# Kernel optimization log

Measured on AMD Instinct MI355X. Metric: run time of the kernel, lower is better.

Reference implementation:

```python
import jax, jax.numpy as jnp
import numpy as np

D_MODEL = 1024
N_HEADS = 16
D_HEAD = D_MODEL // N_HEADS


def setup_inputs() -> dict:
    key = jax.random.key(0)
    ks = jax.random.split(key, 7)
    x = jax.random.normal(ks[0], (1, 4096, D_MODEL), dtype=jnp.float32)
    # torch Linear default init ~ U(-1/sqrt(fan_in), 1/sqrt(fan_in)); small randn is fine for a reference
    Wqkv = jax.random.normal(ks[1], (3 * D_MODEL, D_MODEL), dtype=jnp.float32) * (1.0 / np.sqrt(D_MODEL))
    bqkv = jax.random.normal(ks[2], (3 * D_MODEL,), dtype=jnp.float32) * 0.01
    Wo = jax.random.normal(ks[3], (D_MODEL, D_MODEL), dtype=jnp.float32) * (1.0 / np.sqrt(D_MODEL))
    bo = jax.random.normal(ks[4], (D_MODEL,), dtype=jnp.float32) * 0.01
    wq = jnp.ones((D_HEAD,), dtype=jnp.float32)
    wk = jnp.ones((D_HEAD,), dtype=jnp.float32)
    return {"x": x, "Wqkv": Wqkv, "bqkv": bqkv, "Wo": Wo, "bo": bo, "wq": wq, "wk": wk}


def _rmsnorm(x, w):
    # matches RMSNormRef: mean of squares over last dim, eps added to mean before sqrt
    xf = x.astype(jnp.float32)
    rms = jnp.mean(xf * xf, axis=-1, keepdims=True)
    return (xf / jnp.sqrt(rms + 1e-6) * w.astype(jnp.float32)).astype(x.dtype)


def reference(x, Wqkv, bqkv, Wo, bo, wq, wk):
    b, s, d = x.shape
    qkv = x @ Wqkv.T + bqkv                       # [b, s, 3d]
    q, k, v = jnp.split(qkv, 3, axis=-1)
    q = q.reshape(b, s, N_HEADS, D_HEAD)
    k = k.reshape(b, s, N_HEADS, D_HEAD)
    v = v.reshape(b, s, N_HEADS, D_HEAD)
    q = _rmsnorm(q, wq)
    k = _rmsnorm(k, wk)
    # NOTE: original applies NO 1/sqrt(d_head) scaling and NO causal mask
    qf = q.astype(jnp.float32)
    kf = k.astype(jnp.float32)
    vf = v.astype(jnp.float32)
    attn = jnp.einsum('bqhd,bkhd->bhqk', qf, kf)  # [b, h, s, s] fp32 scores
    attn = jax.nn.softmax(attn, axis=-1)
    z = jnp.einsum('bhqk,bkhd->bqhd', attn, vf).astype(x.dtype)
    z = z.reshape(b, s, d)
    return z @ Wo.T + bo
```

## Files before the change

kernel.cpp:

```cpp
#include <hip/hip_runtime.h>
#include <hip/hip_bf16.h>

typedef __bf16 bf16;
typedef bf16 bf16x8 __attribute__((ext_vector_type(8)));
typedef bf16 bf16x4 __attribute__((ext_vector_type(4)));
typedef float f32x4 __attribute__((ext_vector_type(4)));
typedef float f32x16 __attribute__((ext_vector_type(16)));
typedef unsigned int u32;
typedef u32 u32x4 __attribute__((ext_vector_type(4)));

static constexpr int SEQ    = 4096;
static constexpr int DMODEL = 1024;
static constexpr int NHEADS = 16;
static constexpr int DHEAD  = 64;
static constexpr int QKV3   = 3 * DMODEL;
static constexpr float SMAX = 64.0f;
static constexpr float LOG2E = 1.44269504088896341f;

__device__ inline void gld16(const bf16* g, bf16* l) {
    __builtin_amdgcn_global_load_lds(
        (const __attribute__((address_space(1))) void*)g,
        (__attribute__((address_space(3))) void*)l, 16, 0, 0);
}

__device__ inline bf16x8 load8(const float* src) {
    float4 a = *(const float4*)(src);
    float4 b = *(const float4*)(src + 4);
    bf16x8 r;
    r[0] = (bf16)a.x; r[1] = (bf16)a.y; r[2] = (bf16)a.z; r[3] = (bf16)a.w;
    r[4] = (bf16)b.x; r[5] = (bf16)b.y; r[6] = (bf16)b.z; r[7] = (bf16)b.w;
    return r;
}

__device__ inline f32x16 zero16() {
    f32x16 r;
#pragma unroll
    for (int i = 0; i < 16; ++i) r[i] = 0.f;
    return r;
}

static constexpr size_t NX = (size_t)SEQ * DMODEL;
static constexpr size_t NW = (size_t)QKV3 * DMODEL;
static constexpr size_t NO = (size_t)DMODEL * DMODEL;

__global__ __launch_bounds__(256)
void cvt_all(const float* __restrict__ x, const float* __restrict__ Wqkv,
             const float* __restrict__ Wo, bf16* __restrict__ outbase) {
    const size_t e = ((size_t)blockIdx.x * 256 + threadIdx.x) * 8;
    const float* src;
    if (e < NX)            src = x + e;
    else if (e < NX + NW)  src = Wqkv + (e - NX);
    else                   src = Wo + (e - NX - NW);
    *(bf16x8*)(outbase + e) = load8(src);
}

__global__ __launch_bounds__(256)
void gemm_qkv(const bf16* __restrict__ A, const bf16* __restrict__ W,
              const float* __restrict__ bias, const float* __restrict__ wq,
              const float* __restrict__ wk, bf16* __restrict__ qkv,
              bf16* __restrict__ Vt) {
    __shared__ __align__(16) bf16 As[128 * 32];
    __shared__ __align__(16) bf16 Ws[128 * 32];
    const int tid  = threadIdx.x;
    const int wave = tid >> 6;
    const int ll   = tid & 15;
    const int quad = (tid & 63) >> 4;
    const int wm   = (wave >> 1) * 64;
    const int wn   = (wave & 1) * 64;
    const int m0 = blockIdx.y * 128;
    const int n0 = blockIdx.x * 128;

    f32x4 acc[4][4];
#pragma unroll
    for (int i = 0; i < 4; ++i)
#pragma unroll
        for (int j = 0; j < 4; ++j) acc[i][j] = (f32x4){0.f, 0.f, 0.f, 0.f};

    for (int k0 = 0; k0 < DMODEL; k0 += 32) {
        __syncthreads();
#pragma unroll
        for (int i = 0; i < 2; ++i) {
            const int idx = i * 256 + tid;
            const int row = idx >> 2;
            const int c   = (idx & 3) ^ ((row >> 1) & 3);
            gld16(&A[(size_t)(m0 + row) * DMODEL + k0 + c * 8], As + idx * 8);
            gld16(&W[(size_t)(n0 + row) * DMODEL + k0 + c * 8], Ws + idx * 8);
        }
        __syncthreads();
        bf16x8 af[4], bfr[4];
#pragma unroll
        for (int mi = 0; mi < 4; ++mi) {
            const int row = wm + mi * 16 + ll;
            af[mi] = *(const bf16x8*)(As + (row * 4 + (quad ^ ((ll >> 1) & 3))) * 8);
        }
#pragma unroll
        for (int ni = 0; ni < 4; ++ni) {
            const int row = wn + ni * 16 + ll;
            bfr[ni] = *(const bf16x8*)(Ws + (row * 4 + (quad ^ ((ll >> 1) & 3))) * 8);
        }
#pragma unroll
        for (int mi = 0; mi < 4; ++mi)
#pragma unroll
            for (int ni = 0; ni < 4; ++ni)
                acc[mi][ni] = __builtin_amdgcn_mfma_f32_16x16x32_bf16(
                    af[mi], bfr[ni], acc[mi][ni], 0, 0, 0);
    }

    float bvn[4];
#pragma unroll
    for (int ni = 0; ni < 4; ++ni) bvn[ni] = bias[n0 + wn + ni * 16 + ll];

    const int sect = (n0 + wn) >> 10;
    if (sect < 2) {
        const float* wv = sect ? wk : wq;
        float wvl[4];
#pragma unroll
        for (int ni = 0; ni < 4; ++ni) wvl[ni] = wv[ni * 16 + ll];
#pragma unroll
        for (int mi = 0; mi < 4; ++mi)
#pragma unroll
            for (int r = 0; r < 4; ++r) {
                float xf[4];
                float ss = 0.f;
#pragma unroll
                for (int ni = 0; ni < 4; ++ni) {
                    xf[ni] = (float)(bf16)(acc[mi][ni][r] + bvn[ni]);
                    ss += xf[ni] * xf[ni];
                }
#pragma unroll
                for (int off = 1; off < 16; off <<= 1) ss += __shfl_xor(ss, off);
                const float scale = rsqrtf(ss * (1.0f / 64.0f) + 1e-6f);
                const int row = m0 + wm + mi * 16 + quad * 4 + r;
#pragma unroll
                for (int ni = 0; ni < 4; ++ni)
                    qkv[(size_t)row * QKV3 + n0 + wn + ni * 16 + ll] =
                        (bf16)(xf[ni] * scale * wvl[ni]);
            }
    } else {
        const int h = (n0 + wn - 2 * DMODEL) >> 6;
#pragma unroll
        for (int mi = 0; mi < 4; ++mi) {
            const int kv = m0 + wm + mi * 16 + quad * 4;
#pragma unroll
            for (int ni = 0; ni < 4; ++ni) {
                bf16x4 vv;
#pragma unroll
                for (int r = 0; r < 4; ++r) vv[r] = (bf16)(acc[mi][ni][r] + bvn[ni]);
                *(bf16x4*)(Vt + (size_t)(h * DHEAD + ni * 16 + ll) * SEQ + kv) = vv;
            }
        }
    }
}

__global__ __launch_bounds__(256)
void gemm_out(const bf16* __restrict__ A, const bf16* __restrict__ W,
              const float* __restrict__ bias, float* __restrict__ C) {
    __shared__ __align__(16) bf16 As[128 * 32];
    __shared__ __align__(16) bf16 Ws[64 * 32];
    const int tid  = threadIdx.x;
    const int wave = tid >> 6;
    const int ll   = tid & 15;
    const int quad = (tid & 63) >> 4;
    const int m0 = blockIdx.y * 128;
    const int n0 = blockIdx.x * 64;

    f32x4 acc[2][4];
#pragma unroll
    for (int i = 0; i < 2; ++i)
#pragma unroll
        for (int j = 0; j < 4; ++j) acc[i][j] = (f32x4){0.f, 0.f, 0.f, 0.f};

    for (int k0 = 0; k0 < DMODEL; k0 += 32) {
        __syncthreads();
#pragma unroll
        for (int i = 0; i < 2; ++i) {
            const int idx = i * 256 + tid;
            const int row = idx >> 2;
            const int c   = (idx & 3) ^ ((row >> 1) & 3);
            gld16(&A[(size_t)(m0 + row) * DMODEL + k0 + c * 8], As + idx * 8);
        }
        {
            const int j   = tid;
            const int row = j >> 2;
            const int c   = (j & 3) ^ ((row >> 1) & 3);
            gld16(&W[(size_t)(n0 + row) * DMODEL + k0 + c * 8], Ws + j * 8);
        }
        __syncthreads();
        bf16x8 af[2], bfr[4];
#pragma unroll
        for (int mi = 0; mi < 2; ++mi) {
            const int row = wave * 32 + mi * 16 + ll;
            af[mi] = *(const bf16x8*)(As + (row * 4 + (quad ^ ((ll >> 1) & 3))) * 8);
        }
#pragma unroll
        for (int ni = 0; ni < 4; ++ni) {
            const int row = ni * 16 + ll;
            bfr[ni] = *(const bf16x8*)(Ws + (row * 4 + (quad ^ ((ll >> 1) & 3))) * 8);
        }
#pragma unroll
        for (int mi = 0; mi < 2; ++mi)
#pragma unroll
            for (int ni = 0; ni < 4; ++ni)
                acc[mi][ni] = __builtin_amdgcn_mfma_f32_16x16x32_bf16(
                    af[mi], bfr[ni], acc[mi][ni], 0, 0, 0);
    }
#pragma unroll
    for (int ni = 0; ni < 4; ++ni) {
        const int col = n0 + ni * 16 + ll;
        const float bv = bias[col];
#pragma unroll
        for (int mi = 0; mi < 2; ++mi)
#pragma unroll
            for (int r = 0; r < 4; ++r) {
                const int row = m0 + wave * 32 + mi * 16 + quad * 4 + r;
                C[(size_t)row * DMODEL + col] = acc[mi][ni][r] + bv;
            }
    }
}

template<bool PARTIAL>
__global__ __launch_bounds__(256, 4)
void attn_fwd(const bf16* __restrict__ qkv, const bf16* __restrict__ Vt,
              bf16* __restrict__ z, float* __restrict__ opf,
              float* __restrict__ lsum) {
    __shared__ __align__(16) bf16 KV[2][2][64 * 64];
    float (*Os)[32][36] = (float(*)[32][36])(&KV[0][0][0]);
    bf16* Qs = &KV[1][0][0];

    const int tid  = threadIdx.x;
    const int wave = tid >> 6;
    const int lane = tid & 63;
    const int l31  = lane & 31;
    const int hh   = lane >> 5;
    const int l7   = lane & 7;
    const int head = blockIdx.x;
    const int q0   = blockIdx.y * 128;
    const int half = PARTIAL ? blockIdx.z : 0;
    const int kvbeg = half * (SEQ / 2);
    const int kvlen = PARTIAL ? (SEQ / 2) : SEQ;
    const int nt    = kvlen / 64;

    const bf16* kbase  = qkv + DMODEL + head * DHEAD;
    const bf16* vtbase = Vt + (size_t)head * DHEAD * SEQ;

    auto stage_kv = [&](int buf, int kv0) {
#pragma unroll
        for (int i = 0; i < 2; ++i) {
            const int idx = i * 256 + tid;
            const int row = idx >> 3;
            const int c   = (idx & 7) ^ (row & 7);
            gld16(kbase + (size_t)(kv0 + row) * QKV3 + c * 8, &KV[buf][0][0] + idx * 8);
            gld16(vtbase + (size_t)row * SEQ + kv0 + c * 8, &KV[buf][1][0] + idx * 8);
        }
    };

#pragma unroll
    for (int i = 0; i < 4; ++i) {
        const int idx = i * 256 + tid;
        const int row = idx >> 3;
        const int c   = (idx & 7) ^ (row & 7);
        gld16(qkv + (size_t)(q0 + row) * QKV3 + head * DHEAD + c * 8, Qs + idx * 8);
    }
    stage_kv(0, kvbeg);
    __syncthreads();

    bf16x8 qf[4];
#pragma unroll
    for (int kd = 0; kd < 4; ++kd)
        qf[kd] = *(const bf16x8*)(Qs + ((wave * 32 + l31) * 8 + ((kd * 2 + hh) ^ l7)) * 8);
    __syncthreads();

    f32x16 o[2];
    o[0] = zero16();
    o[1] = zero16();
    float lpa[4] = {0.f, 0.f, 0.f, 0.f};

    int cur = 0;
    for (int t = 0; t < nt; ++t) {
        if (t + 1 < nt) stage_kv(cur ^ 1, kvbeg + (t + 1) * 64);
        const bf16* Ks  = &KV[cur][0][0];
        const bf16* VTs = &KV[cur][1][0];

        f32x16 st0 = zero16(), st1 = zero16();
        __builtin_amdgcn_s_setprio(1);
#pragma unroll
        for (int kd = 0; kd < 4; ++kd) {
            bf16x8 kf = *(const bf16x8*)(Ks + ((l31) * 8 + ((kd * 2 + hh) ^ l7)) * 8);
            st0 = __builtin_amdgcn_mfma_f32_32x32x16_bf16(kf, qf[kd], st0, 0, 0, 0);
        }
#pragma unroll
        for (int kd = 0; kd < 4; ++kd) {
            bf16x8 kf = *(const bf16x8*)(Ks + ((32 + l31) * 8 + ((kd * 2 + hh) ^ l7)) * 8);
            st1 = __builtin_amdgcn_mfma_f32_32x32x16_bf16(kf, qf[kd], st1, 0, 0, 0);
        }
        __builtin_amdgcn_s_setprio(0);

#pragma unroll
        for (int kvt = 0; kvt < 2; ++kvt) {
            const f32x16 stv = kvt ? st1 : st0;
            float pf[16];
#pragma unroll
            for (int r = 0; r < 16; ++r)
                pf[r] = __builtin_amdgcn_exp2f(
                    __builtin_fmaf(stv[r], LOG2E, -SMAX * LOG2E));
#pragma unroll
            for (int r = 0; r < 16; ++r) lpa[r & 3] += pf[r];
#pragma unroll
            for (int cc = 0; cc < 2; ++cc) {
                u32 a1, b1, a2, b2;
                asm("v_cvt_pk_bf16_f32 %0, %1, %2" : "=v"(a1) : "v"(pf[8 * cc + 0]), "v"(pf[8 * cc + 1]));
                asm("v_cvt_pk_bf16_f32 %0, %1, %2" : "=v"(b1) : "v"(pf[8 * cc + 4]), "v"(pf[8 * cc + 5]));
                asm("v_cvt_pk_bf16_f32 %0, %1, %2" : "=v"(a2) : "v"(pf[8 * cc + 2]), "v"(pf[8 * cc + 3]));
                asm("v_cvt_pk_bf16_f32 %0, %1, %2" : "=v"(b2) : "v"(pf[8 * cc + 6]), "v"(pf[8 * cc + 7]));
                asm("v_permlane32_swap_b32 %0, %1" : "+v"(a1), "+v"(b1));
                asm("v_permlane32_swap_b32 %0, %1" : "+v"(a2), "+v"(b2));
                u32x4 w;
                w[0] = a1; w[1] = a2; w[2] = b1; w[3] = b2;
                const bf16x8 bp = *(const bf16x8*)&w;
                const int c = kvt * 2 + cc;
                __builtin_amdgcn_s_setprio(1);
#pragma unroll
                for (int dt = 0; dt < 2; ++dt) {
                    bf16x8 vf = *(const bf16x8*)(
                        VTs + ((dt * 32 + l31) * 8 + ((c * 2 + hh) ^ l7)) * 8);
                    o[dt] = __builtin_amdgcn_mfma_f32_32x32x16_bf16(vf, bp, o[dt], 0, 0, 0);
                }
                __builtin_amdgcn_s_setprio(0);
            }
        }
        __syncthreads();
        cur ^= 1;
    }

    float lp = (lpa[0] + lpa[1]) + (lpa[2] + lpa[3]);
    lp += __shfl_xor(lp, 32);
    const int qrow = q0 + wave * 32 + l31;
    if (PARTIAL) {
        if (lane < 32) lsum[((size_t)half * SEQ + qrow) * NHEADS + head] = lp;
    }
    const float inv = PARTIAL ? 1.0f : 1.0f / lp;

#pragma unroll
    for (int dt = 0; dt < 2; ++dt) {
#pragma unroll
        for (int r = 0; r < 16; ++r) {
            const int dl = (r & 3) + 8 * (r >> 2) + 4 * hh;
            Os[wave][l31][dl] = o[dt][r] * inv;
        }
#pragma unroll
        for (int it = 0; it < 4; ++it) {
            const int qr  = it * 8 + (lane >> 3);
            const int dl2 = (lane & 7) * 4;
            const f32x4 v = *(const f32x4*)(&Os[wave][qr][dl2]);
            const int row = q0 + wave * 32 + qr;
            const int col = head * DHEAD + dt * 32 + dl2;
            if (PARTIAL) {
                *(f32x4*)(opf + ((size_t)half * SEQ + row) * DMODEL + col) = v;
            } else {
                bf16x4 ov;
                ov[0] = (bf16)v[0]; ov[1] = (bf16)v[1];
                ov[2] = (bf16)v[2]; ov[3] = (bf16)v[3];
                *(bf16x4*)(z + (size_t)row * DMODEL + col) = ov;
            }
        }
    }
}

__global__ __launch_bounds__(256)
void combine_halves(const float* __restrict__ opf, const float* __restrict__ lsum,
                    bf16* __restrict__ z) {
    const int row = blockIdx.x;
    const int c   = threadIdx.x * 4;
    const int head = c >> 6;
    const float l = lsum[(size_t)row * NHEADS + head] +
                    lsum[((size_t)SEQ + row) * NHEADS + head];
    const float4 o0 = *(const float4*)(opf + (size_t)row * DMODEL + c);
    const float4 o1 = *(const float4*)(opf + ((size_t)SEQ + row) * DMODEL + c);
    bf16x4 out;
    out[0] = (bf16)((o0.x + o1.x) / l);
    out[1] = (bf16)((o0.y + o1.y) / l);
    out[2] = (bf16)((o0.z + o1.z) / l);
    out[3] = (bf16)((o0.w + o1.w) / l);
    *(bf16x4*)(z + (size_t)row * DMODEL + c) = out;
}

extern "C" void kernel_launch(void* const* d_in, const int* in_sizes, int n_in,
                              void* d_out, int out_size, void* d_ws, size_t ws_size,
                              hipStream_t stream) {
    const float* x    = (const float*)d_in[0];
    const float* Wqkv = (const float*)d_in[1];
    const float* bqkv = (const float*)d_in[2];
    const float* Wo   = (const float*)d_in[3];
    const float* bo   = (const float*)d_in[4];
    const float* wq   = (const float*)d_in[5];
    const float* wk   = (const float*)d_in[6];
    float* out = (float*)d_out;

    bf16* qkv  = (bf16*)d_ws;
    bf16* z    = qkv + (size_t)SEQ * QKV3;
    bf16* Vt   = z + (size_t)SEQ * DMODEL;
    bf16* xb   = Vt + (size_t)NHEADS * DHEAD * SEQ;
    bf16* Wqb  = xb + NX;
    bf16* Wob  = Wqb + NW;
    bf16* endb = Wob + NO;
    float* opf  = (float*)endb;
    float* lsum = opf + (size_t)2 * SEQ * DMODEL;
    const size_t need = (size_t)((char*)(lsum + (size_t)2 * SEQ * NHEADS) - (char*)d_ws);
    const bool split = ws_size >= need;

    cvt_all<<<dim3((NX + NW + NO) / 2048), 256, 0, stream>>>(x, Wqkv, Wo, xb);

    gemm_qkv<<<dim3(QKV3 / 128, SEQ / 128), 256, 0, stream>>>(
        xb, Wqb, bqkv, wq, wk, qkv, Vt);

    if (split) {
        attn_fwd<true><<<dim3(NHEADS, SEQ / 128, 2), 256, 0, stream>>>(
            qkv, Vt, z, opf, lsum);
        combine_halves<<<dim3(SEQ), 256, 0, stream>>>(opf, lsum, z);
    } else {
        attn_fwd<false><<<dim3(NHEADS, SEQ / 128, 1), 256, 0, stream>>>(
            qkv, Vt, z, nullptr, nullptr);
    }

    gemm_out<<<dim3(DMODEL / 64, SEQ / 128), 256, 0, stream>>>(z, Wob, bo, out);
}
```

Baseline: 241.4 us.

## Double query rows per attention block to reuse each K/V tile across two Q sub-tiles

```diff
diff --git a/kernel.cpp b/kernel.cpp
--- a/kernel.cpp
+++ b/kernel.cpp
@@ -219,13 +219,13 @@
 }
 
 template<bool PARTIAL>
-__global__ __launch_bounds__(256, 4)
+__global__ __launch_bounds__(256, 2)
 void attn_fwd(const bf16* __restrict__ qkv, const bf16* __restrict__ Vt,
               bf16* __restrict__ z, float* __restrict__ opf,
               float* __restrict__ lsum) {
     __shared__ __align__(16) bf16 KV[2][2][64 * 64];
     float (*Os)[32][36] = (float(*)[32][36])(&KV[0][0][0]);
-    bf16* Qs = &KV[1][0][0];
+    bf16* Qs = &KV[0][0][0];
 
     const int tid  = threadIdx.x;
     const int wave = tid >> 6;
@@ -234,7 +234,7 @@
     const int hh   = lane >> 5;
     const int l7   = lane & 7;
     const int head = blockIdx.x;
-    const int q0   = blockIdx.y * 128;
+    const int q0   = blockIdx.y * 256;
     const int half = PARTIAL ? blockIdx.z : 0;
     const int kvbeg = half * (SEQ / 2);
     const int kvlen = PARTIAL ? (SEQ / 2) : SEQ;
@@ -255,25 +255,29 @@
     };
 
 #pragma unroll
-    for (int i = 0; i < 4; ++i) {
+    for (int i = 0; i < 8; ++i) {
         const int idx = i * 256 + tid;
         const int row = idx >> 3;
         const int c   = (idx & 7) ^ (row & 7);
         gld16(qkv + (size_t)(q0 + row) * QKV3 + head * DHEAD + c * 8, Qs + idx * 8);
     }
+    __syncthreads();
+    bf16x8 qf[4][2];
+#pragma unroll
+    for (int kd = 0; kd < 4; ++kd)
+#pragma unroll
+        for (int qs = 0; qs < 2; ++qs) {
+            const int row = wave * 64 + qs * 32 + l31;
+            qf[kd][qs] = *(const bf16x8*)(Qs + (row * 8 + ((kd * 2 + hh) ^ l7)) * 8);
+        }
+    __syncthreads();
     stage_kv(0, kvbeg);
     __syncthreads();
 
-    bf16x8 qf[4];
-#pragma unroll
-    for (int kd = 0; kd < 4; ++kd)
-        qf[kd] = *(const bf16x8*)(Qs + ((wave * 32 + l31) * 8 + ((kd * 2 + hh) ^ l7)) * 8);
-    __syncthreads();
-
-    f32x16 o[2];
-    o[0] = zero16();
-    o[1] = zero16();
-    float lpa[4] = {0.f, 0.f, 0.f, 0.f};
+    f32x16 o[2][2];
+    o[0][0] = zero16(); o[0][1] = zero16();
+    o[1][0] = zero16(); o[1][1] = zero16();
+    float lpa[2][4] = {{0.f, 0.f, 0.f, 0.f}, {0.f, 0.f, 0.f, 0.f}};
 
     int cur = 0;
     for (int t = 0; t < nt; ++t) {
@@ -281,49 +285,61 @@
         const bf16* Ks  = &KV[cur][0][0];
         const bf16* VTs = &KV[cur][1][0];
 
-        f32x16 st0 = zero16(), st1 = zero16();
-        __builtin_amdgcn_s_setprio(1);
-#pragma unroll
-        for (int kd = 0; kd < 4; ++kd) {
-            bf16x8 kf = *(const bf16x8*)(Ks + ((l31) * 8 + ((kd * 2 + hh) ^ l7)) * 8);
-            st0 = __builtin_amdgcn_mfma_f32_32x32x16_bf16(kf, qf[kd], st0, 0, 0, 0);
-        }
-#pragma unroll
-        for (int kd = 0; kd < 4; ++kd) {
-            bf16x8 kf = *(const bf16x8*)(Ks + ((32 + l31) * 8 + ((kd * 2 + hh) ^ l7)) * 8);
-            st1 = __builtin_amdgcn_mfma_f32_32x32x16_bf16(kf, qf[kd], st1, 0, 0, 0);
-        }
-        __builtin_amdgcn_s_setprio(0);
-
 #pragma unroll
         for (int kvt = 0; kvt < 2; ++kvt) {
-            const f32x16 stv = kvt ? st1 : st0;
-            float pf[16];
+            f32x16 st0 = zero16(), st1 = zero16();
+            __builtin_amdgcn_s_setprio(1);
+#pragma unroll
+            for (int kd = 0; kd < 4; ++kd) {
+                bf16x8 kf = *(const bf16x8*)(
+                    Ks + ((kvt * 32 + l31) * 8 + ((kd * 2 + hh) ^ l7)) * 8);
+                st0 = __builtin_amdgcn_mfma_f32_32x32x16_bf16(kf, qf[kd][0], st0, 0, 0, 0);
+                st1 = __builtin_amdgcn_mfma_f32_32x32x16_bf16(kf, qf[kd][1], st1, 0, 0, 0);
+            }
+            __builtin_amdgcn_s_setprio(0);
+
+            float pf0[16], pf1[16];
 #pragma unroll
             for (int r = 0; r < 16; ++r)
-                pf[r] = __builtin_amdgcn_exp2f(
-                    __builtin_fmaf(stv[r], LOG2E, -SMAX * LOG2E));
-#pragma unroll
-            for (int r = 0; r < 16; ++r) lpa[r & 3] += pf[r];
+                pf0[r] = __builtin_amdgcn_exp2f(
+                    __builtin_fmaf(st0[r], LOG2E, -SMAX * LOG2E));
+#pragma unroll
+            for (int r = 0; r < 16; ++r)
+                pf1[r] = __builtin_amdgcn_exp2f(
+                    __builtin_fmaf(st1[r], LOG2E, -SMAX * LOG2E));
+#pragma unroll
+            for (int r = 0; r < 16; ++r) lpa[0][r & 3] += pf0[r];
+#pragma unroll
+            for (int r = 0; r < 16; ++r) lpa[1][r & 3] += pf1[r];
+
 #pragma unroll
             for (int cc = 0; cc < 2; ++cc) {
-                u32 a1, b1, a2, b2;
-                asm("v_cvt_pk_bf16_f32 %0, %1, %2" : "=v"(a1) : "v"(pf[8 * cc + 0]), "v"(pf[8 * cc + 1]));
-                asm("v_cvt_pk_bf16_f32 %0, %1, %2" : "=v"(b1) : "v"(pf[8 * cc + 4]), "v"(pf[8 * cc + 5]));
-                asm("v_cvt_pk_bf16_f32 %0, %1, %2" : "=v"(a2) : "v"(pf[8 * cc + 2]), "v"(pf[8 * cc + 3]));
-                asm("v_cvt_pk_bf16_f32 %0, %1, %2" : "=v"(b2) : "v"(pf[8 * cc + 6]), "v"(pf[8 * cc + 7]));
+                u32 a1, b1, a2, b2, a3, b3, a4, b4;
+                asm("v_cvt_pk_bf16_f32 %0, %1, %2" : "=v"(a1) : "v"(pf0[8 * cc + 0]), "v"(pf0[8 * cc + 1]));
+                asm("v_cvt_pk_bf16_f32 %0, %1, %2" : "=v"(b1) : "v"(pf0[8 * cc + 4]), "v"(pf0[8 * cc + 5]));
+                asm("v_cvt_pk_bf16_f32 %0, %1, %2" : "=v"(a2) : "v"(pf0[8 * cc + 2]), "v"(pf0[8 * cc + 3]));
+                asm("v_cvt_pk_bf16_f32 %0, %1, %2" : "=v"(b2) : "v"(pf0[8 * cc + 6]), "v"(pf0[8 * cc + 7]));
                 asm("v_permlane32_swap_b32 %0, %1" : "+v"(a1), "+v"(b1));
                 asm("v_permlane32_swap_b32 %0, %1" : "+v"(a2), "+v"(b2));
-                u32x4 w;
-                w[0] = a1; w[1] = a2; w[2] = b1; w[3] = b2;
-                const bf16x8 bp = *(const bf16x8*)&w;
+                asm("v_cvt_pk_bf16_f32 %0, %1, %2" : "=v"(a3) : "v"(pf1[8 * cc + 0]), "v"(pf1[8 * cc + 1]));
+                asm("v_cvt_pk_bf16_f32 %0, %1, %2" : "=v"(b3) : "v"(pf1[8 * cc + 4]), "v"(pf1[8 * cc + 5]));
+                asm("v_cvt_pk_bf16_f32 %0, %1, %2" : "=v"(a4) : "v"(pf1[8 * cc + 2]), "v"(pf1[8 * cc + 3]));
+                asm("v_cvt_pk_bf16_f32 %0, %1, %2" : "=v"(b4) : "v"(pf1[8 * cc + 6]), "v"(pf1[8 * cc + 7]));
+                asm("v_permlane32_swap_b32 %0, %1" : "+v"(a3), "+v"(b3));
+                asm("v_permlane32_swap_b32 %0, %1" : "+v"(a4), "+v"(b4));
+                u32x4 w0, w1;
+                w0[0] = a1; w0[1] = a2; w0[2] = b1; w0[3] = b2;
+                w1[0] = a3; w1[1] = a4; w1[2] = b3; w1[3] = b4;
+                const bf16x8 bp0 = *(const bf16x8*)&w0;
+                const bf16x8 bp1 = *(const bf16x8*)&w1;
                 const int c = kvt * 2 + cc;
                 __builtin_amdgcn_s_setprio(1);
 #pragma unroll
                 for (int dt = 0; dt < 2; ++dt) {
                     bf16x8 vf = *(const bf16x8*)(
                         VTs + ((dt * 32 + l31) * 8 + ((c * 2 + hh) ^ l7)) * 8);
-                    o[dt] = __builtin_amdgcn_mfma_f32_32x32x16_bf16(vf, bp, o[dt], 0, 0, 0);
+                    o[dt][0] = __builtin_amdgcn_mfma_f32_32x32x16_bf16(vf, bp0, o[dt][0], 0, 0, 0);
+                    o[dt][1] = __builtin_amdgcn_mfma_f32_32x32x16_bf16(vf, bp1, o[dt][1], 0, 0, 0);
                 }
                 __builtin_amdgcn_s_setprio(0);
             }
@@ -332,35 +348,38 @@
         cur ^= 1;
     }
 
-    float lp = (lpa[0] + lpa[1]) + (lpa[2] + lpa[3]);
-    lp += __shfl_xor(lp, 32);
-    const int qrow = q0 + wave * 32 + l31;
-    if (PARTIAL) {
-        if (lane < 32) lsum[((size_t)half * SEQ + qrow) * NHEADS + head] = lp;
-    }
-    const float inv = PARTIAL ? 1.0f : 1.0f / lp;
-
-#pragma unroll
-    for (int dt = 0; dt < 2; ++dt) {
-#pragma unroll
-        for (int r = 0; r < 16; ++r) {
-            const int dl = (r & 3) + 8 * (r >> 2) + 4 * hh;
-            Os[wave][l31][dl] = o[dt][r] * inv;
-        }
-#pragma unroll
-        for (int it = 0; it < 4; ++it) {
-            const int qr  = it * 8 + (lane >> 3);
-            const int dl2 = (lane & 7) * 4;
-            const f32x4 v = *(const f32x4*)(&Os[wave][qr][dl2]);
-            const int row = q0 + wave * 32 + qr;
-            const int col = head * DHEAD + dt * 32 + dl2;
-            if (PARTIAL) {
-                *(f32x4*)(opf + ((size_t)half * SEQ + row) * DMODEL + col) = v;
-            } else {
-                bf16x4 ov;
-                ov[0] = (bf16)v[0]; ov[1] = (bf16)v[1];
-                ov[2] = (bf16)v[2]; ov[3] = (bf16)v[3];
-                *(bf16x4*)(z + (size_t)row * DMODEL + col) = ov;
+#pragma unroll
+    for (int qs = 0; qs < 2; ++qs) {
+        float lp = (lpa[qs][0] + lpa[qs][1]) + (lpa[qs][2] + lpa[qs][3]);
+        lp += __shfl_xor(lp, 32);
+        const int qrow = q0 + wave * 64 + qs * 32 + l31;
+        if (PARTIAL) {
+            if (lane < 32) lsum[((size_t)half * SEQ + qrow) * NHEADS + head] = lp;
+        }
+        const float inv = PARTIAL ? 1.0f : 1.0f / lp;
+
+#pragma unroll
+        for (int dt = 0; dt < 2; ++dt) {
+#pragma unroll
+            for (int r = 0; r < 16; ++r) {
+                const int dl = (r & 3) + 8 * (r >> 2) + 4 * hh;
+                Os[wave][l31][dl] = o[dt][qs][r] * inv;
+            }
+#pragma unroll
+            for (int it = 0; it < 4; ++it) {
+                const int qr  = it * 8 + (lane >> 3);
+                const int dl2 = (lane & 7) * 4;
+                const f32x4 v = *(const f32x4*)(&Os[wave][qr][dl2]);
+                const int row = q0 + wave * 64 + qs * 32 + qr;
+                const int col = head * DHEAD + dt * 32 + dl2;
+                if (PARTIAL) {
+                    *(f32x4*)(opf + ((size_t)half * SEQ + row) * DMODEL + col) = v;
+                } else {
+                    bf16x4 ov;
+                    ov[0] = (bf16)v[0]; ov[1] = (bf16)v[1];
+                    ov[2] = (bf16)v[2]; ov[3] = (bf16)v[3];
+                    *(bf16x4*)(z + (size_t)row * DMODEL + col) = ov;
+                }
             }
         }
     }
@@ -414,11 +433,11 @@
         xb, Wqb, bqkv, wq, wk, qkv, Vt);
 
     if (split) {
-        attn_fwd<true><<<dim3(NHEADS, SEQ / 128, 2), 256, 0, stream>>>(
+        attn_fwd<true><<<dim3(NHEADS, SEQ / 256, 2), 256, 0, stream>>>(
             qkv, Vt, z, opf, lsum);
         combine_halves<<<dim3(SEQ), 256, 0, stream>>>(opf, lsum, z);
     } else {
-        attn_fwd<false><<<dim3(NHEADS, SEQ / 128, 1), 256, 0, stream>>>(
+        attn_fwd<false><<<dim3(NHEADS, SEQ / 256, 1), 256, 0, stream>>>(
             qkv, Vt, z, nullptr, nullptr);
     }
 
```

After: 234.7 us. 2.8% less time.
